# Performance work log

Measured on AMD Instinct MI355X. Metric: run time of the kernel, lower is better.

The kernel has to match this reference:

```python
import jax, jax.numpy as jnp
import numpy as np

B, T, K = 256, 64, 512


def setup_inputs() -> dict:
    key = jax.random.key(0)
    k1, k2, k3, k4, k5 = jax.random.split(key, 5)
    return {
        "x": jax.random.uniform(k1, (B, T), dtype=jnp.float32),          # soft binary evidence
        "prior_w": jax.random.normal(k2, (K,), dtype=jnp.float32),
        "emission_w": jax.random.normal(k3, (K, 2), dtype=jnp.float32),
        "coeff": jax.random.normal(k4, (K, K), dtype=jnp.float32),
        "bias": jax.random.normal(k5, (K, K), dtype=jnp.float32),
    }


def reference(x, prior_w, emission_w, coeff, bias):
    # emission: per-row softmax of [K,2] raw weights (TF loops rows; equivalent to axis=1 softmax)
    emission = jax.nn.softmax(emission_w, axis=1)  # [K, 2]

    def evidence(h, xt):
        # h: [B,K] (or broadcastable [1,K]); xt: [B]
        aug = jnp.stack([1.0 - xt, xt], axis=1)          # [B, 2]
        e = aug @ emission.T                             # [B, K]
        p = h * e                                        # [B, K]
        return p / jnp.sum(p, axis=1, keepdims=True)     # row-normalize (get_normalized_pr)

    prior = jax.nn.softmax(prior_w)                      # [K]
    post0 = evidence(prior[None, :], x[:, 0])            # [B, K]

    def step(post, xt):
        # transition_raw[i,j,k] = post[i,j]*coeff[j,k] + bias[j,k]
        raw = post[:, :, None] * coeff[None, :, :] + bias[None, :, :]   # [B, K, K]
        trans = jax.nn.softmax(raw, axis=2)              # get_normalized_pr_with_batch
        pbe = jnp.einsum('ij,ijk->ik', post, trans)      # [B, K]
        return evidence(pbe, xt), None

    post, _ = jax.lax.scan(step, post0, x[:, 1:].T)      # scan over time steps 1..T-1
    return post
```

## Files before the change

kernel.cpp:

```cpp
#include <hip/hip_runtime.h>

#define KDIM 512
#define TDIM 64
#define NWAVE 16
#define BLOCK 1024
#define LOG2E 1.4426950408889634f

typedef float v2f __attribute__((ext_vector_type(2)));

#define WS_B2     0
#define WS_XCHG   (KDIM * KDIM)
#define WS_FLAGS  (WS_XCHG + 128 * 2 * 2 * 1024)
#define WS_FLOATS (WS_FLAGS + 256)

__device__ __forceinline__ float fast_exp2(float v) { return __builtin_amdgcn_exp2f(v); }
__device__ __forceinline__ float fast_rcp(float v)  { return __builtin_amdgcn_rcpf(v); }

__global__ __launch_bounds__(256) void prefold_kernel(
    const float* __restrict__ bias, float* __restrict__ b2)
{
    const int i = blockIdx.x * 256 + threadIdx.x;
    const float4 b = ((const float4*)bias)[i];
    ((float4*)b2)[i] = make_float4(b.x * LOG2E, b.y * LOG2E, b.z * LOG2E, b.w * LOG2E);
}

__device__ __forceinline__ float wave_reduce_sum(float v) {
    #pragma unroll
    for (int off = 1; off < 64; off <<= 1)
        v += __shfl_xor(v, off, 64);
    return v;
}

__global__ __launch_bounds__(BLOCK)
__attribute__((amdgpu_waves_per_eu(4, 4)))
void hmm_pair_kernel(
    const float* __restrict__ x,
    const float* __restrict__ prior_w,
    const float* __restrict__ emission_w,
    const float* __restrict__ coeff,
    float* __restrict__ ws,
    float* __restrict__ out)
{
    __shared__ float post[2][KDIM];
    __shared__ float em0s[KDIM];
    __shared__ float emds[KDIM];
    __shared__ float part[NWAVE][2][KDIM];
    __shared__ float rtmp[NWAVE];
    __shared__ float xs[2][TDIM];

    const int gid  = blockIdx.x;
    const int pair = gid & 127;
    const int h    = gid >> 7;
    const int b0   = 2 * pair;
    const int tid  = threadIdx.x;
    const int lane = tid & 63;
    const int wv   = tid >> 6;
    const int k0   = 4 * lane;
    const int u    = tid >> 9;
    const int k    = tid & 511;

    const float* bb = ws + WS_B2;
    int* flags   = (int*)(ws + WS_FLAGS);
    int* my_flag = flags + (pair * 2 + h);
    int* pr_flag = flags + (pair * 2 + (1 - h));
    float* my_slot = ws + WS_XCHG + (size_t)(pair * 2 + h) * 2048;
    float* pr_slot = ws + WS_XCHG + (size_t)(pair * 2 + (1 - h)) * 2048;

    if (tid < 2 * TDIM) xs[tid >> 6][tid & 63] = x[(b0 + (tid >> 6)) * TDIM + (tid & 63)];
    if (tid < KDIM) {
        const float w0 = emission_w[2 * tid + 0];
        const float w1 = emission_w[2 * tid + 1];
        const float e0 = 1.0f / (1.0f + fast_exp2((w1 - w0) * LOG2E));
        em0s[tid] = e0;
        emds[tid] = 1.0f - 2.0f * e0;
    }
    __syncthreads();

    {
        const float x0 = xs[u][0];
        float v = fast_exp2(prior_w[k] * LOG2E) * fmaf(x0, emds[k], em0s[k]);
        float s = wave_reduce_sum(v);
        if (lane == 0) rtmp[wv] = s;
        __syncthreads();
        const float* rb = &rtmp[u * 8];
        const float tot = ((rb[0] + rb[1]) + (rb[2] + rb[3]))
                        + ((rb[4] + rb[5]) + (rb[6] + rb[7]));
        post[u][k] = v * fast_rcp(tot);
        __syncthreads();
    }

    for (int t = 1; t < TDIM; ++t) {
        v2f acc[2][4];
        #pragma unroll
        for (int uu = 0; uu < 2; ++uu)
            #pragma unroll
            for (int q = 0; q < 4; ++q) acc[uu][q] = (v2f){0.0f, 0.0f};

        const float* pc = coeff + (size_t)(h * 256 + wv) * KDIM + k0;
        const float* pb = bb    + (size_t)(h * 256 + wv) * KDIM + k0;

        #pragma unroll 1
        for (int i = 0; i < 8; ++i) {
            const int jA = h * 256 + wv + 32 * i;
            const float4 cA0 = *(const float4*)pc;
            const float4 cA1 = *(const float4*)(pc + 256);
            const float4 cB0 = *(const float4*)(pc + 16 * KDIM);
            const float4 cB1 = *(const float4*)(pc + 16 * KDIM + 256);
            const float4 bA0 = *(const float4*)pb;
            const float4 bA1 = *(const float4*)(pb + 256);
            const float4 bB0 = *(const float4*)(pb + 16 * KDIM);
            const float4 bB1 = *(const float4*)(pb + 16 * KDIM + 256);
            pc += 32 * KDIM; pb += 32 * KDIM;

            const v2f cav[4] = {{cA0.x, cA0.y}, {cA0.z, cA0.w}, {cA1.x, cA1.y}, {cA1.z, cA1.w}};
            const v2f cbv[4] = {{cB0.x, cB0.y}, {cB0.z, cB0.w}, {cB1.x, cB1.y}, {cB1.z, cB1.w}};
            const v2f bav[4] = {{bA0.x, bA0.y}, {bA0.z, bA0.w}, {bA1.x, bA1.y}, {bA1.z, bA1.w}};
            const v2f bbv[4] = {{bB0.x, bB0.y}, {bB0.z, bB0.w}, {bB1.x, bB1.y}, {bB1.z, bB1.w}};

            float p[2][2];
            p[0][0] = post[0][jA]; p[0][1] = post[0][jA + 16];
            p[1][0] = post[1][jA]; p[1][1] = post[1][jA + 16];

            v2f ev[2][2][4];
            float s[4];
            #pragma unroll
            for (int uu = 0; uu < 2; ++uu) {
                const float pAL = p[uu][0] * LOG2E;
                const float pBL = p[uu][1] * LOG2E;
                const v2f pAv = {pAL, pAL};
                const v2f pBv = {pBL, pBL};
                #pragma unroll
                for (int q = 0; q < 4; ++q) {
                    const v2f aA = __builtin_elementwise_fma(pAv, cav[q], bav[q]);
                    const v2f aB = __builtin_elementwise_fma(pBv, cbv[q], bbv[q]);
                    v2f eA, eB;
                    eA.x = fast_exp2(aA.x); eA.y = fast_exp2(aA.y);
                    eB.x = fast_exp2(aB.x); eB.y = fast_exp2(aB.y);
                    ev[uu][0][q] = eA;
                    ev[uu][1][q] = eB;
                }
                const v2f tA = (ev[uu][0][0] + ev[uu][0][1]) + (ev[uu][0][2] + ev[uu][0][3]);
                const v2f tB = (ev[uu][1][0] + ev[uu][1][1]) + (ev[uu][1][2] + ev[uu][1][3]);
                s[uu * 2 + 0] = tA.x + tA.y;
                s[uu * 2 + 1] = tB.x + tB.y;
            }
            #pragma unroll
            for (int off = 1; off < 64; off <<= 1) {
                s[0] += __shfl_xor(s[0], off, 64);
                s[1] += __shfl_xor(s[1], off, 64);
                s[2] += __shfl_xor(s[2], off, 64);
                s[3] += __shfl_xor(s[3], off, 64);
            }
            #pragma unroll
            for (int uu = 0; uu < 2; ++uu) {
                const float scA = p[uu][0] * fast_rcp(s[uu * 2 + 0]);
                const float scB = p[uu][1] * fast_rcp(s[uu * 2 + 1]);
                const v2f scAv = {scA, scA};
                const v2f scBv = {scB, scB};
                #pragma unroll
                for (int q = 0; q < 4; ++q) {
                    acc[uu][q] = __builtin_elementwise_fma(scAv, ev[uu][0][q], acc[uu][q]);
                    acc[uu][q] = __builtin_elementwise_fma(scBv, ev[uu][1][q], acc[uu][q]);
                }
            }
        }

        *(float4*)(&part[wv][0][k0])       = make_float4(acc[0][0].x, acc[0][0].y, acc[0][1].x, acc[0][1].y);
        *(float4*)(&part[wv][0][256 + k0]) = make_float4(acc[0][2].x, acc[0][2].y, acc[0][3].x, acc[0][3].y);
        *(float4*)(&part[wv][1][k0])       = make_float4(acc[1][0].x, acc[1][0].y, acc[1][1].x, acc[1][1].y);
        *(float4*)(&part[wv][1][256 + k0]) = make_float4(acc[1][2].x, acc[1][2].y, acc[1][3].x, acc[1][3].y);
        __syncthreads();

        float pbe = 0.0f;
        #pragma unroll
        for (int w2 = 0; w2 < NWAVE; ++w2) pbe += part[w2][u][k];

        float* slot = my_slot + (t & 1) * 1024;
        __hip_atomic_store(&slot[tid], pbe, __ATOMIC_RELAXED, __HIP_MEMORY_SCOPE_AGENT);
        __syncthreads();
        if (tid == 0) {
            __hip_atomic_store(my_flag, t, __ATOMIC_RELEASE, __HIP_MEMORY_SCOPE_AGENT);
            int f = __hip_atomic_load(pr_flag, __ATOMIC_ACQUIRE, __HIP_MEMORY_SCOPE_AGENT);
            while (f < t) {
                __builtin_amdgcn_s_sleep(1);
                f = __hip_atomic_load(pr_flag, __ATOMIC_ACQUIRE, __HIP_MEMORY_SCOPE_AGENT);
            }
        }
        __syncthreads();
        const float* pslot = pr_slot + (t & 1) * 1024;
        const float other = __hip_atomic_load(&pslot[tid], __ATOMIC_RELAXED, __HIP_MEMORY_SCOPE_AGENT);

        float v = (pbe + other) * fmaf(xs[u][t], emds[k], em0s[k]);
        float s = wave_reduce_sum(v);
        if (lane == 0) rtmp[wv] = s;
        __syncthreads();
        const float* rb = &rtmp[u * 8];
        const float tot = ((rb[0] + rb[1]) + (rb[2] + rb[3]))
                        + ((rb[4] + rb[5]) + (rb[6] + rb[7]));
        post[u][k] = v * fast_rcp(tot);
        __syncthreads();
    }

    if (tid < KDIM) out[(size_t)(b0 + h) * KDIM + tid] = post[h][tid];
}

__global__ __launch_bounds__(BLOCK)
__attribute__((amdgpu_waves_per_eu(4, 4)))
void hmm_forward_kernel(
    const float* __restrict__ x, const float* __restrict__ prior_w,
    const float* __restrict__ emission_w, const float* __restrict__ coeff,
    const float* __restrict__ bias, float* __restrict__ out)
{
    __shared__ float post[KDIM];
    __shared__ float em0s[KDIM];
    __shared__ float emds[KDIM];
    __shared__ float part[NWAVE][KDIM];
    __shared__ float rtmp[NWAVE];
    __shared__ float xs[TDIM];

    const int b = blockIdx.x, tid = threadIdx.x, lane = tid & 63, wv = tid >> 6;
    const int k0 = 4 * lane;

    if (tid < TDIM) xs[tid] = x[b * TDIM + tid];
    if (tid < KDIM) {
        const float w0 = emission_w[2 * tid + 0];
        const float w1 = emission_w[2 * tid + 1];
        const float e0 = 1.0f / (1.0f + fast_exp2((w1 - w0) * LOG2E));
        em0s[tid] = e0;
        emds[tid] = 1.0f - 2.0f * e0;
    }
    __syncthreads();
    {
        const float x0 = xs[0];
        float v = 0.0f;
        if (tid < KDIM)
            v = fast_exp2(prior_w[tid] * LOG2E) * fmaf(x0, emds[tid], em0s[tid]);
        float s = wave_reduce_sum(v);
        if (lane == 0) rtmp[wv] = s;
        __syncthreads();
        if (wv == 0) {
            float t2 = (lane < NWAVE) ? rtmp[lane] : 0.0f;
            #pragma unroll
            for (int off = 1; off < NWAVE; off <<= 1) t2 += __shfl_xor(t2, off, 64);
            if (lane == 0) rtmp[0] = t2;
        }
        __syncthreads();
        const float rn = fast_rcp(rtmp[0]);
        if (tid < KDIM) post[tid] = v * rn;
        __syncthreads();
    }
    for (int t = 1; t < TDIM; ++t) {
        float acc[8];
        #pragma unroll
        for (int i = 0; i < 8; ++i) acc[i] = 0.0f;
        const float* cA = coeff + (size_t)wv * KDIM + k0;
        const float* bA = bias  + (size_t)wv * KDIM + k0;
        #pragma unroll 1
        for (int i = 0; i < 16; ++i) {
            const float4 cA0 = *(const float4*)cA;
            const float4 cA1 = *(const float4*)(cA + 256);
            const float4 cB0 = *(const float4*)(cA + 16 * KDIM);
            const float4 cB1 = *(const float4*)(cA + 16 * KDIM + 256);
            const float4 bA0 = *(const float4*)bA;
            const float4 bA1 = *(const float4*)(bA + 256);
            const float4 bB0 = *(const float4*)(bA + 16 * KDIM);
            const float4 bB1 = *(const float4*)(bA + 16 * KDIM + 256);
            cA += 32 * KDIM; bA += 32 * KDIM;
            const float pA = post[wv + 32 * i];
            const float pB = post[wv + 16 + 32 * i];
            const float eA0 = fast_exp2(fmaf(pA, cA0.x, bA0.x) * LOG2E);
            const float eA1 = fast_exp2(fmaf(pA, cA0.y, bA0.y) * LOG2E);
            const float eA2 = fast_exp2(fmaf(pA, cA0.z, bA0.z) * LOG2E);
            const float eA3 = fast_exp2(fmaf(pA, cA0.w, bA0.w) * LOG2E);
            const float eA4 = fast_exp2(fmaf(pA, cA1.x, bA1.x) * LOG2E);
            const float eA5 = fast_exp2(fmaf(pA, cA1.y, bA1.y) * LOG2E);
            const float eA6 = fast_exp2(fmaf(pA, cA1.z, bA1.z) * LOG2E);
            const float eA7 = fast_exp2(fmaf(pA, cA1.w, bA1.w) * LOG2E);
            const float eB0 = fast_exp2(fmaf(pB, cB0.x, bB0.x) * LOG2E);
            const float eB1 = fast_exp2(fmaf(pB, cB0.y, bB0.y) * LOG2E);
            const float eB2 = fast_exp2(fmaf(pB, cB0.z, bB0.z) * LOG2E);
            const float eB3 = fast_exp2(fmaf(pB, cB0.w, bB0.w) * LOG2E);
            const float eB4 = fast_exp2(fmaf(pB, cB1.x, bB1.x) * LOG2E);
            const float eB5 = fast_exp2(fmaf(pB, cB1.y, bB1.y) * LOG2E);
            const float eB6 = fast_exp2(fmaf(pB, cB1.z, bB1.z) * LOG2E);
            const float eB7 = fast_exp2(fmaf(pB, cB1.w, bB1.w) * LOG2E);
            float sA = ((eA0 + eA1) + (eA2 + eA3)) + ((eA4 + eA5) + (eA6 + eA7));
            float sB = ((eB0 + eB1) + (eB2 + eB3)) + ((eB4 + eB5) + (eB6 + eB7));
            #pragma unroll
            for (int off = 1; off < 64; off <<= 1) {
                sA += __shfl_xor(sA, off, 64);
                sB += __shfl_xor(sB, off, 64);
            }
            const float scA = pA * fast_rcp(sA);
            const float scB = pB * fast_rcp(sB);
            acc[0] = fmaf(scA, eA0, acc[0]); acc[0] = fmaf(scB, eB0, acc[0]);
            acc[1] = fmaf(scA, eA1, acc[1]); acc[1] = fmaf(scB, eB1, acc[1]);
            acc[2] = fmaf(scA, eA2, acc[2]); acc[2] = fmaf(scB, eB2, acc[2]);
            acc[3] = fmaf(scA, eA3, acc[3]); acc[3] = fmaf(scB, eB3, acc[3]);
            acc[4] = fmaf(scA, eA4, acc[4]); acc[4] = fmaf(scB, eB4, acc[4]);
            acc[5] = fmaf(scA, eA5, acc[5]); acc[5] = fmaf(scB, eB5, acc[5]);
            acc[6] = fmaf(scA, eA6, acc[6]); acc[6] = fmaf(scB, eB6, acc[6]);
            acc[7] = fmaf(scA, eA7, acc[7]); acc[7] = fmaf(scB, eB7, acc[7]);
        }
        *(float4*)(&part[wv][k0])       = make_float4(acc[0], acc[1], acc[2], acc[3]);
        *(float4*)(&part[wv][256 + k0]) = make_float4(acc[4], acc[5], acc[6], acc[7]);
        __syncthreads();
        float v = 0.0f;
        if (tid < KDIM) {
            float pbe = 0.0f;
            #pragma unroll
            for (int w2 = 0; w2 < NWAVE; ++w2) pbe += part[w2][tid];
            v = pbe * fmaf(xs[t], emds[tid], em0s[tid]);
        }
        float s = wave_reduce_sum(v);
        if (lane == 0) rtmp[wv] = s;
        __syncthreads();
        if (wv == 0) {
            float t2 = (lane < NWAVE) ? rtmp[lane] : 0.0f;
            #pragma unroll
            for (int off = 1; off < NWAVE; off <<= 1) t2 += __shfl_xor(t2, off, 64);
            if (lane == 0) rtmp[0] = t2;
        }
        __syncthreads();
        const float rn = fast_rcp(rtmp[0]);
        if (tid < KDIM) post[tid] = v * rn;
        __syncthreads();
    }
    if (tid < KDIM) out[b * KDIM + tid] = post[tid];
}

extern "C" void kernel_launch(void* const* d_in, const int* in_sizes, int n_in,
                              void* d_out, int out_size, void* d_ws, size_t ws_size,
                              hipStream_t stream) {
    const float* x          = (const float*)d_in[0];
    const float* prior_w    = (const float*)d_in[1];
    const float* emission_w = (const float*)d_in[2];
    const float* coeff      = (const float*)d_in[3];
    const float* bias       = (const float*)d_in[4];
    float* out              = (float*)d_out;

    if (ws_size >= (size_t)WS_FLOATS * sizeof(float)) {
        float* ws = (float*)d_ws;
        hipLaunchKernelGGL(prefold_kernel, dim3(KDIM * KDIM / 4 / 256), dim3(256),
                           0, stream, bias, ws + WS_B2);
        hipLaunchKernelGGL(hmm_pair_kernel, dim3(256), dim3(BLOCK), 0, stream,
                           x, prior_w, emission_w, coeff, ws, out);
    } else {
        hipLaunchKernelGGL(hmm_forward_kernel, dim3(256), dim3(BLOCK), 0, stream,
                           x, prior_w, emission_w, coeff, bias, out);
    }
}
```

Measured before the change: 1.134 ms.

## Split each batch row across two 512-thread blocks and use DPP reductions

The paired kernel previously had one 1024-thread block handle half of the j-range for two batch rows. Now each of 512 blocks handles one batch row and half of the j-range, and exchanges partial sums with a partner block through flags in the workspace. This doubles the grid so more CUs take part, and halves per-block register and LDS pressure. Wave reductions now use DPP row shifts instead of a full shuffle-xor ladder. The cost is that coeff and bias are re-read per row instead of shared across two rows, and twice as many cross-block flag syncs run per step.

```diff
diff --git a/kernel.cpp b/kernel.cpp
--- a/kernel.cpp
+++ b/kernel.cpp
@@ -2,19 +2,47 @@
 
 #define KDIM 512
 #define TDIM 64
-#define NWAVE 16
-#define BLOCK 1024
+#define BLOCK 512
+#define NWAVE 8
 #define LOG2E 1.4426950408889634f
 
 typedef float v2f __attribute__((ext_vector_type(2)));
 
 #define WS_B2     0
 #define WS_XCHG   (KDIM * KDIM)
-#define WS_FLAGS  (WS_XCHG + 128 * 2 * 2 * 1024)
-#define WS_FLOATS (WS_FLAGS + 256)
+#define WS_FLAGS  (WS_XCHG + 512 * 1024)
+#define WS_FLOATS (WS_FLAGS + 512)
 
 __device__ __forceinline__ float fast_exp2(float v) { return __builtin_amdgcn_exp2f(v); }
 __device__ __forceinline__ float fast_rcp(float v)  { return __builtin_amdgcn_rcpf(v); }
+
+template <int CTRL>
+__device__ __forceinline__ float dpp_add(float v) {
+    const int p = __builtin_amdgcn_update_dpp(
+        0, __builtin_bit_cast(int, v), CTRL, 0xF, 0xF, true);
+    return v + __builtin_bit_cast(float, p);
+}
+
+__device__ __forceinline__ float row_sum64(float v) {
+    v = dpp_add<0x121>(v);
+    v = dpp_add<0x122>(v);
+    v = dpp_add<0x124>(v);
+    v = dpp_add<0x128>(v);
+    v += __shfl_xor(v, 16, 64);
+    v += __shfl_xor(v, 32, 64);
+    return v;
+}
+
+__device__ __forceinline__ void row_sum64_x2(float& a, float& b) {
+    a = dpp_add<0x121>(a); b = dpp_add<0x121>(b);
+    a = dpp_add<0x122>(a); b = dpp_add<0x122>(b);
+    a = dpp_add<0x124>(a); b = dpp_add<0x124>(b);
+    a = dpp_add<0x128>(a); b = dpp_add<0x128>(b);
+    float ta = __shfl_xor(a, 16, 64), tb = __shfl_xor(b, 16, 64);
+    a += ta; b += tb;
+    ta = __shfl_xor(a, 32, 64); tb = __shfl_xor(b, 32, 64);
+    a += ta; b += tb;
+}
 
 __global__ __launch_bounds__(256) void prefold_kernel(
     const float* __restrict__ bias, float* __restrict__ b2)
@@ -22,13 +50,6 @@
     const int i = blockIdx.x * 256 + threadIdx.x;
     const float4 b = ((const float4*)bias)[i];
     ((float4*)b2)[i] = make_float4(b.x * LOG2E, b.y * LOG2E, b.z * LOG2E, b.w * LOG2E);
-}
-
-__device__ __forceinline__ float wave_reduce_sum(float v) {
-    #pragma unroll
-    for (int off = 1; off < 64; off <<= 1)
-        v += __shfl_xor(v, off, 64);
-    return v;
 }
 
 __global__ __launch_bounds__(BLOCK)
@@ -41,33 +62,30 @@
     float* __restrict__ ws,
     float* __restrict__ out)
 {
-    __shared__ float post[2][KDIM];
+    __shared__ float post[KDIM];
     __shared__ float em0s[KDIM];
     __shared__ float emds[KDIM];
-    __shared__ float part[NWAVE][2][KDIM];
+    __shared__ float part[NWAVE][KDIM];
     __shared__ float rtmp[NWAVE];
-    __shared__ float xs[2][TDIM];
+    __shared__ float xs[TDIM];
 
     const int gid  = blockIdx.x;
-    const int pair = gid & 127;
-    const int h    = gid >> 7;
-    const int b0   = 2 * pair;
+    const int b    = gid & 255;
+    const int h    = gid >> 8;
     const int tid  = threadIdx.x;
     const int lane = tid & 63;
     const int wv   = tid >> 6;
     const int k0   = 4 * lane;
-    const int u    = tid >> 9;
-    const int k    = tid & 511;
 
     const float* bb = ws + WS_B2;
     int* flags   = (int*)(ws + WS_FLAGS);
-    int* my_flag = flags + (pair * 2 + h);
-    int* pr_flag = flags + (pair * 2 + (1 - h));
-    float* my_slot = ws + WS_XCHG + (size_t)(pair * 2 + h) * 2048;
-    float* pr_slot = ws + WS_XCHG + (size_t)(pair * 2 + (1 - h)) * 2048;
-
-    if (tid < 2 * TDIM) xs[tid >> 6][tid & 63] = x[(b0 + (tid >> 6)) * TDIM + (tid & 63)];
-    if (tid < KDIM) {
+    int* my_flag = flags + (b * 2 + h);
+    int* pr_flag = flags + (b * 2 + (1 - h));
+    float* my_slot = ws + WS_XCHG + (size_t)(b * 2 + h) * 1024;
+    float* pr_slot = ws + WS_XCHG + (size_t)(b * 2 + (1 - h)) * 1024;
+
+    if (tid < TDIM) xs[tid] = x[b * TDIM + tid];
+    {
         const float w0 = emission_w[2 * tid + 0];
         const float w1 = emission_w[2 * tid + 1];
         const float e0 = 1.0f / (1.0f + fast_exp2((w1 - w0) * LOG2E));
@@ -77,105 +95,83 @@
     __syncthreads();
 
     {
-        const float x0 = xs[u][0];
-        float v = fast_exp2(prior_w[k] * LOG2E) * fmaf(x0, emds[k], em0s[k]);
-        float s = wave_reduce_sum(v);
+        const float x0 = xs[0];
+        float v = fast_exp2(prior_w[tid] * LOG2E) * fmaf(x0, emds[tid], em0s[tid]);
+        const float s = row_sum64(v);
         if (lane == 0) rtmp[wv] = s;
         __syncthreads();
-        const float* rb = &rtmp[u * 8];
-        const float tot = ((rb[0] + rb[1]) + (rb[2] + rb[3]))
-                        + ((rb[4] + rb[5]) + (rb[6] + rb[7]));
-        post[u][k] = v * fast_rcp(tot);
+        const float tot = ((rtmp[0] + rtmp[1]) + (rtmp[2] + rtmp[3]))
+                        + ((rtmp[4] + rtmp[5]) + (rtmp[6] + rtmp[7]));
+        post[tid] = v * fast_rcp(tot);
         __syncthreads();
     }
 
     for (int t = 1; t < TDIM; ++t) {
-        v2f acc[2][4];
+        v2f acc[4];
         #pragma unroll
-        for (int uu = 0; uu < 2; ++uu)
-            #pragma unroll
-            for (int q = 0; q < 4; ++q) acc[uu][q] = (v2f){0.0f, 0.0f};
+        for (int q = 0; q < 4; ++q) acc[q] = (v2f){0.0f, 0.0f};
 
         const float* pc = coeff + (size_t)(h * 256 + wv) * KDIM + k0;
         const float* pb = bb    + (size_t)(h * 256 + wv) * KDIM + k0;
 
         #pragma unroll 1
-        for (int i = 0; i < 8; ++i) {
-            const int jA = h * 256 + wv + 32 * i;
+        for (int i = 0; i < 16; ++i) {
+            const int jA = h * 256 + wv + 16 * i;
             const float4 cA0 = *(const float4*)pc;
             const float4 cA1 = *(const float4*)(pc + 256);
-            const float4 cB0 = *(const float4*)(pc + 16 * KDIM);
-            const float4 cB1 = *(const float4*)(pc + 16 * KDIM + 256);
+            const float4 cB0 = *(const float4*)(pc + 8 * KDIM);
+            const float4 cB1 = *(const float4*)(pc + 8 * KDIM + 256);
             const float4 bA0 = *(const float4*)pb;
             const float4 bA1 = *(const float4*)(pb + 256);
-            const float4 bB0 = *(const float4*)(pb + 16 * KDIM);
-            const float4 bB1 = *(const float4*)(pb + 16 * KDIM + 256);
-            pc += 32 * KDIM; pb += 32 * KDIM;
+            const float4 bB0 = *(const float4*)(pb + 8 * KDIM);
+            const float4 bB1 = *(const float4*)(pb + 8 * KDIM + 256);
+            pc += 16 * KDIM; pb += 16 * KDIM;
 
             const v2f cav[4] = {{cA0.x, cA0.y}, {cA0.z, cA0.w}, {cA1.x, cA1.y}, {cA1.z, cA1.w}};
             const v2f cbv[4] = {{cB0.x, cB0.y}, {cB0.z, cB0.w}, {cB1.x, cB1.y}, {cB1.z, cB1.w}};
             const v2f bav[4] = {{bA0.x, bA0.y}, {bA0.z, bA0.w}, {bA1.x, bA1.y}, {bA1.z, bA1.w}};
             const v2f bbv[4] = {{bB0.x, bB0.y}, {bB0.z, bB0.w}, {bB1.x, bB1.y}, {bB1.z, bB1.w}};
 
-            float p[2][2];
-            p[0][0] = post[0][jA]; p[0][1] = post[0][jA + 16];
-            p[1][0] = post[1][jA]; p[1][1] = post[1][jA + 16];
-
-            v2f ev[2][2][4];
-            float s[4];
+            const float pA = post[jA];
+            const float pB = post[jA + 8];
+            const float pAL = pA * LOG2E;
+            const float pBL = pB * LOG2E;
+            const v2f pAv = {pAL, pAL};
+            const v2f pBv = {pBL, pBL};
+
+            v2f eA[4], eB[4];
             #pragma unroll
-            for (int uu = 0; uu < 2; ++uu) {
-                const float pAL = p[uu][0] * LOG2E;
-                const float pBL = p[uu][1] * LOG2E;
-                const v2f pAv = {pAL, pAL};
-                const v2f pBv = {pBL, pBL};
-                #pragma unroll
-                for (int q = 0; q < 4; ++q) {
-                    const v2f aA = __builtin_elementwise_fma(pAv, cav[q], bav[q]);
-                    const v2f aB = __builtin_elementwise_fma(pBv, cbv[q], bbv[q]);
-                    v2f eA, eB;
-                    eA.x = fast_exp2(aA.x); eA.y = fast_exp2(aA.y);
-                    eB.x = fast_exp2(aB.x); eB.y = fast_exp2(aB.y);
-                    ev[uu][0][q] = eA;
-                    ev[uu][1][q] = eB;
-                }
-                const v2f tA = (ev[uu][0][0] + ev[uu][0][1]) + (ev[uu][0][2] + ev[uu][0][3]);
-                const v2f tB = (ev[uu][1][0] + ev[uu][1][1]) + (ev[uu][1][2] + ev[uu][1][3]);
-                s[uu * 2 + 0] = tA.x + tA.y;
-                s[uu * 2 + 1] = tB.x + tB.y;
+            for (int q = 0; q < 4; ++q) {
+                const v2f aA = __builtin_elementwise_fma(pAv, cav[q], bav[q]);
+                const v2f aB = __builtin_elementwise_fma(pBv, cbv[q], bbv[q]);
+                eA[q].x = fast_exp2(aA.x); eA[q].y = fast_exp2(aA.y);
+                eB[q].x = fast_exp2(aB.x); eB[q].y = fast_exp2(aB.y);
             }
+            const v2f tA = (eA[0] + eA[1]) + (eA[2] + eA[3]);
+            const v2f tB = (eB[0] + eB[1]) + (eB[2] + eB[3]);
+            float sA = tA.x + tA.y;
+            float sB = tB.x + tB.y;
+            row_sum64_x2(sA, sB);
+
+            const float scA = pA * fast_rcp(sA);
+            const float scB = pB * fast_rcp(sB);
+            const v2f scAv = {scA, scA};
+            const v2f scBv = {scB, scB};
             #pragma unroll
-            for (int off = 1; off < 64; off <<= 1) {
-                s[0] += __shfl_xor(s[0], off, 64);
-                s[1] += __shfl_xor(s[1], off, 64);
-                s[2] += __shfl_xor(s[2], off, 64);
-                s[3] += __shfl_xor(s[3], off, 64);
-            }
-            #pragma unroll
-            for (int uu = 0; uu < 2; ++uu) {
-                const float scA = p[uu][0] * fast_rcp(s[uu * 2 + 0]);
-                const float scB = p[uu][1] * fast_rcp(s[uu * 2 + 1]);
-                const v2f scAv = {scA, scA};
-                const v2f scBv = {scB, scB};
-                #pragma unroll
-                for (int q = 0; q < 4; ++q) {
-                    acc[uu][q] = __builtin_elementwise_fma(scAv, ev[uu][0][q], acc[uu][q]);
-                    acc[uu][q] = __builtin_elementwise_fma(scBv, ev[uu][1][q], acc[uu][q]);
-                }
+            for (int q = 0; q < 4; ++q) {
+                acc[q] = __builtin_elementwise_fma(scAv, eA[q], acc[q]);
+                acc[q] = __builtin_elementwise_fma(scBv, eB[q], acc[q]);
             }
         }
 
-        *(float4*)(&part[wv][0][k0])       = make_float4(acc[0][0].x, acc[0][0].y, acc[0][1].x, acc[0][1].y);
-        *(float4*)(&part[wv][0][256 + k0]) = make_float4(acc[0][2].x, acc[0][2].y, acc[0][3].x, acc[0][3].y);
-        *(float4*)(&part[wv][1][k0])       = make_float4(acc[1][0].x, acc[1][0].y, acc[1][1].x, acc[1][1].y);
-        *(float4*)(&part[wv][1][256 + k0]) = make_float4(acc[1][2].x, acc[1][2].y, acc[1][3].x, acc[1][3].y);
-        __syncthreads();
-
-        float pbe = 0.0f;
-        #pragma unroll
-        for (int w2 = 0; w2 < NWAVE; ++w2) pbe += part[w2][u][k];
-
-        float* slot = my_slot + (t & 1) * 1024;
+        *(float4*)(&part[wv][k0])       = make_float4(acc[0].x, acc[0].y, acc[1].x, acc[1].y);
+        *(float4*)(&part[wv][256 + k0]) = make_float4(acc[2].x, acc[2].y, acc[3].x, acc[3].y);
+        __syncthreads();
+
+        float pbe = ((part[0][tid] + part[1][tid]) + (part[2][tid] + part[3][tid]))
+                  + ((part[4][tid] + part[5][tid]) + (part[6][tid] + part[7][tid]));
+
+        float* slot = my_slot + (t & 1) * 512;
         __hip_atomic_store(&slot[tid], pbe, __ATOMIC_RELAXED, __HIP_MEMORY_SCOPE_AGENT);
         __syncthreads();
         if (tid == 0) {
@@ -187,24 +183,23 @@
             }
         }
         __syncthreads();
-        const float* pslot = pr_slot + (t & 1) * 1024;
+        const float* pslot = pr_slot + (t & 1) * 512;
         const float other = __hip_atomic_load(&pslot[tid], __ATOMIC_RELAXED, __HIP_MEMORY_SCOPE_AGENT);
 
-        float v = (pbe + other) * fmaf(xs[u][t], emds[k], em0s[k]);
-        float s = wave_reduce_sum(v);
+        float v = (pbe + other) * fmaf(xs[t], emds[tid], em0s[tid]);
+        const float s = row_sum64(v);
         if (lane == 0) rtmp[wv] = s;
         __syncthreads();
-        const float* rb = &rtmp[u * 8];
-        const float tot = ((rb[0] + rb[1]) + (rb[2] + rb[3]))
-                        + ((rb[4] + rb[5]) + (rb[6] + rb[7]));
-        post[u][k] = v * fast_rcp(tot);
-        __syncthreads();
-    }
-
-    if (tid < KDIM) out[(size_t)(b0 + h) * KDIM + tid] = post[h][tid];
-}
-
-__global__ __launch_bounds__(BLOCK)
+        const float tot = ((rtmp[0] + rtmp[1]) + (rtmp[2] + rtmp[3]))
+                        + ((rtmp[4] + rtmp[5]) + (rtmp[6] + rtmp[7]));
+        post[tid] = v * fast_rcp(tot);
+        __syncthreads();
+    }
+
+    if (h == 0) out[(size_t)b * KDIM + tid] = post[tid];
+}
+
+__global__ __launch_bounds__(1024)
 __attribute__((amdgpu_waves_per_eu(4, 4)))
 void hmm_forward_kernel(
     const float* __restrict__ x, const float* __restrict__ prior_w,
@@ -214,8 +209,8 @@
     __shared__ float post[KDIM];
     __shared__ float em0s[KDIM];
     __shared__ float emds[KDIM];
-    __shared__ float part[NWAVE][KDIM];
-    __shared__ float rtmp[NWAVE];
+    __shared__ float part[16][KDIM];
+    __shared__ float rtmp[16];
     __shared__ float xs[TDIM];
 
     const int b = blockIdx.x, tid = threadIdx.x, lane = tid & 63, wv = tid >> 6;
@@ -235,18 +230,13 @@
         float v = 0.0f;
         if (tid < KDIM)
             v = fast_exp2(prior_w[tid] * LOG2E) * fmaf(x0, emds[tid], em0s[tid]);
-        float s = wave_reduce_sum(v);
+        float s = row_sum64(v);
         if (lane == 0) rtmp[wv] = s;
         __syncthreads();
-        if (wv == 0) {
-            float t2 = (lane < NWAVE) ? rtmp[lane] : 0.0f;
-            #pragma unroll
-            for (int off = 1; off < NWAVE; off <<= 1) t2 += __shfl_xor(t2, off, 64);
-            if (lane == 0) rtmp[0] = t2;
-        }
-        __syncthreads();
-        const float rn = fast_rcp(rtmp[0]);
-        if (tid < KDIM) post[tid] = v * rn;
+        float tot = 0.0f;
+        #pragma unroll
+        for (int w2 = 0; w2 < 16; ++w2) tot += rtmp[w2];
+        if (tid < KDIM) post[tid] = v * fast_rcp(tot);
         __syncthreads();
     }
     for (int t = 1; t < TDIM; ++t) {
@@ -286,11 +276,7 @@
             const float eB7 = fast_exp2(fmaf(pB, cB1.w, bB1.w) * LOG2E);
             float sA = ((eA0 + eA1) + (eA2 + eA3)) + ((eA4 + eA5) + (eA6 + eA7));
             float sB = ((eB0 + eB1) + (eB2 + eB3)) + ((eB4 + eB5) + (eB6 + eB7));
-            #pragma unroll
-            for (int off = 1; off < 64; off <<= 1) {
-                sA += __shfl_xor(sA, off, 64);
-                sB += __shfl_xor(sB, off, 64);
-            }
+            row_sum64_x2(sA, sB);
             const float scA = pA * fast_rcp(sA);
             const float scB = pB * fast_rcp(sB);
             acc[0] = fmaf(scA, eA0, acc[0]); acc[0] = fmaf(scB, eB0, acc[0]);
@@ -309,21 +295,16 @@
         if (tid < KDIM) {
             float pbe = 0.0f;
             #pragma unroll
-            for (int w2 = 0; w2 < NWAVE; ++w2) pbe += part[w2][tid];
+            for (int w2 = 0; w2 < 16; ++w2) pbe += part[w2][tid];
             v = pbe * fmaf(xs[t], emds[tid], em0s[tid]);
         }
-        float s = wave_reduce_sum(v);
+        float s = row_sum64(v);
         if (lane == 0) rtmp[wv] = s;
         __syncthreads();
-        if (wv == 0) {
-            float t2 = (lane < NWAVE) ? rtmp[lane] : 0.0f;
-            #pragma unroll
-            for (int off = 1; off < NWAVE; off <<= 1) t2 += __shfl_xor(t2, off, 64);
-            if (lane == 0) rtmp[0] = t2;
-        }
-        __syncthreads();
-        const float rn = fast_rcp(rtmp[0]);
-        if (tid < KDIM) post[tid] = v * rn;
+        float tot = 0.0f;
+        #pragma unroll
+        for (int w2 = 0; w2 < 16; ++w2) tot += rtmp[w2];
+        if (tid < KDIM) post[tid] = v * fast_rcp(tot);
         __syncthreads();
     }
     if (tid < KDIM) out[b * KDIM + tid] = post[tid];
@@ -343,10 +324,10 @@
         float* ws = (float*)d_ws;
         hipLaunchKernelGGL(prefold_kernel, dim3(KDIM * KDIM / 4 / 256), dim3(256),
                            0, stream, bias, ws + WS_B2);
-        hipLaunchKernelGGL(hmm_pair_kernel, dim3(256), dim3(BLOCK), 0, stream,
+        hipLaunchKernelGGL(hmm_pair_kernel, dim3(512), dim3(BLOCK), 0, stream,
                            x, prior_w, emission_w, coeff, ws, out);
     } else {
-        hipLaunchKernelGGL(hmm_forward_kernel, dim3(256), dim3(BLOCK), 0, stream,
+        hipLaunchKernelGGL(hmm_forward_kernel, dim3(256), dim3(1024), 0, stream,
                            x, prior_w, emission_w, coeff, bias, out);
     }
 }
```

New measurement: 3.812 ms. 236% more time.

## Use DPP row reductions and per-wave cross-block flags instead of block barriers

Applied to the files above, without the earlier changes.

Wave-wide sums now use DPP row-shift adds for the first four reduction steps and shuffles only for the last two, which shortens the reduction chain inside the hot softmax loop. The pair-exchange handshake switches to one flag per wave: each wave publishes and polls its own flag with relaxed loads and an acquire fence. This removes the two block-wide barriers around the cross-block exchange. It adds more flag traffic and spinning waves, and the flag workspace is enlarged to hold the per-wave flags.

```diff
diff --git a/kernel.cpp b/kernel.cpp
--- a/kernel.cpp
+++ b/kernel.cpp
@@ -10,11 +10,45 @@
 
 #define WS_B2     0
 #define WS_XCHG   (KDIM * KDIM)
-#define WS_FLAGS  (WS_XCHG + 128 * 2 * 2 * 1024)
-#define WS_FLOATS (WS_FLAGS + 256)
+#define WS_FLAGS  (WS_XCHG + 256 * 2048)
+#define WS_FLOATS (WS_FLAGS + 128 * 2 * 16)
 
 __device__ __forceinline__ float fast_exp2(float v) { return __builtin_amdgcn_exp2f(v); }
 __device__ __forceinline__ float fast_rcp(float v)  { return __builtin_amdgcn_rcpf(v); }
+
+template <int CTRL>
+__device__ __forceinline__ float dpp_add(float v) {
+    const int p = __builtin_amdgcn_update_dpp(
+        0, __builtin_bit_cast(int, v), CTRL, 0xF, 0xF, true);
+    return v + __builtin_bit_cast(float, p);
+}
+
+__device__ __forceinline__ float row_sum64(float v) {
+    v = dpp_add<0x121>(v);
+    v = dpp_add<0x122>(v);
+    v = dpp_add<0x124>(v);
+    v = dpp_add<0x128>(v);
+    v += __shfl_xor(v, 16, 64);
+    v += __shfl_xor(v, 32, 64);
+    return v;
+}
+
+__device__ __forceinline__ void row_sum64_x4(float* s) {
+    #pragma unroll
+    for (int q = 0; q < 4; ++q) s[q] = dpp_add<0x121>(s[q]);
+    #pragma unroll
+    for (int q = 0; q < 4; ++q) s[q] = dpp_add<0x122>(s[q]);
+    #pragma unroll
+    for (int q = 0; q < 4; ++q) s[q] = dpp_add<0x124>(s[q]);
+    #pragma unroll
+    for (int q = 0; q < 4; ++q) s[q] = dpp_add<0x128>(s[q]);
+    float t0 = __shfl_xor(s[0], 16, 64), t1 = __shfl_xor(s[1], 16, 64);
+    float t2 = __shfl_xor(s[2], 16, 64), t3 = __shfl_xor(s[3], 16, 64);
+    s[0] += t0; s[1] += t1; s[2] += t2; s[3] += t3;
+    t0 = __shfl_xor(s[0], 32, 64); t1 = __shfl_xor(s[1], 32, 64);
+    t2 = __shfl_xor(s[2], 32, 64); t3 = __shfl_xor(s[3], 32, 64);
+    s[0] += t0; s[1] += t1; s[2] += t2; s[3] += t3;
+}
 
 __global__ __launch_bounds__(256) void prefold_kernel(
     const float* __restrict__ bias, float* __restrict__ b2)
@@ -22,13 +56,6 @@
     const int i = blockIdx.x * 256 + threadIdx.x;
     const float4 b = ((const float4*)bias)[i];
     ((float4*)b2)[i] = make_float4(b.x * LOG2E, b.y * LOG2E, b.z * LOG2E, b.w * LOG2E);
-}
-
-__device__ __forceinline__ float wave_reduce_sum(float v) {
-    #pragma unroll
-    for (int off = 1; off < 64; off <<= 1)
-        v += __shfl_xor(v, off, 64);
-    return v;
 }
 
 __global__ __launch_bounds__(BLOCK)
@@ -61,8 +88,8 @@
 
     const float* bb = ws + WS_B2;
     int* flags   = (int*)(ws + WS_FLAGS);
-    int* my_flag = flags + (pair * 2 + h);
-    int* pr_flag = flags + (pair * 2 + (1 - h));
+    int* my_flag = flags + ((pair * 2 + h) * 16 + wv);
+    int* pr_flag = flags + ((pair * 2 + (1 - h)) * 16 + wv);
     float* my_slot = ws + WS_XCHG + (size_t)(pair * 2 + h) * 2048;
     float* pr_slot = ws + WS_XCHG + (size_t)(pair * 2 + (1 - h)) * 2048;
 
@@ -79,7 +106,7 @@
     {
         const float x0 = xs[u][0];
         float v = fast_exp2(prior_w[k] * LOG2E) * fmaf(x0, emds[k], em0s[k]);
-        float s = wave_reduce_sum(v);
+        const float s = row_sum64(v);
         if (lane == 0) rtmp[wv] = s;
         __syncthreads();
         const float* rb = &rtmp[u * 8];
@@ -144,13 +171,8 @@
                 s[uu * 2 + 0] = tA.x + tA.y;
                 s[uu * 2 + 1] = tB.x + tB.y;
             }
-            #pragma unroll
-            for (int off = 1; off < 64; off <<= 1) {
-                s[0] += __shfl_xor(s[0], off, 64);
-                s[1] += __shfl_xor(s[1], off, 64);
-                s[2] += __shfl_xor(s[2], off, 64);
-                s[3] += __shfl_xor(s[3], off, 64);
-            }
+            row_sum64_x4(s);
+
             #pragma unroll
             for (int uu = 0; uu < 2; ++uu) {
                 const float scA = p[uu][0] * fast_rcp(s[uu * 2 + 0]);
@@ -177,21 +199,19 @@
 
         float* slot = my_slot + (t & 1) * 1024;
         __hip_atomic_store(&slot[tid], pbe, __ATOMIC_RELAXED, __HIP_MEMORY_SCOPE_AGENT);
-        __syncthreads();
-        if (tid == 0) {
+        if (lane == 0)
             __hip_atomic_store(my_flag, t, __ATOMIC_RELEASE, __HIP_MEMORY_SCOPE_AGENT);
-            int f = __hip_atomic_load(pr_flag, __ATOMIC_ACQUIRE, __HIP_MEMORY_SCOPE_AGENT);
-            while (f < t) {
-                __builtin_amdgcn_s_sleep(1);
-                f = __hip_atomic_load(pr_flag, __ATOMIC_ACQUIRE, __HIP_MEMORY_SCOPE_AGENT);
-            }
+        int f = __hip_atomic_load(pr_flag, __ATOMIC_RELAXED, __HIP_MEMORY_SCOPE_AGENT);
+        while (f < t) {
+            __builtin_amdgcn_s_sleep(4);
+            f = __hip_atomic_load(pr_flag, __ATOMIC_RELAXED, __HIP_MEMORY_SCOPE_AGENT);
         }
-        __syncthreads();
+        __builtin_amdgcn_fence(__ATOMIC_ACQUIRE, "agent");
         const float* pslot = pr_slot + (t & 1) * 1024;
         const float other = __hip_atomic_load(&pslot[tid], __ATOMIC_RELAXED, __HIP_MEMORY_SCOPE_AGENT);
 
         float v = (pbe + other) * fmaf(xs[u][t], emds[k], em0s[k]);
-        float s = wave_reduce_sum(v);
+        const float s = row_sum64(v);
         if (lane == 0) rtmp[wv] = s;
         __syncthreads();
         const float* rb = &rtmp[u * 8];
@@ -204,7 +224,7 @@
     if (tid < KDIM) out[(size_t)(b0 + h) * KDIM + tid] = post[h][tid];
 }
 
-__global__ __launch_bounds__(BLOCK)
+__global__ __launch_bounds__(1024)
 __attribute__((amdgpu_waves_per_eu(4, 4)))
 void hmm_forward_kernel(
     const float* __restrict__ x, const float* __restrict__ prior_w,
@@ -214,8 +234,8 @@
     __shared__ float post[KDIM];
     __shared__ float em0s[KDIM];
     __shared__ float emds[KDIM];
-    __shared__ float part[NWAVE][KDIM];
-    __shared__ float rtmp[NWAVE];
+    __shared__ float part[16][KDIM];
+    __shared__ float rtmp[16];
     __shared__ float xs[TDIM];
 
     const int b = blockIdx.x, tid = threadIdx.x, lane = tid & 63, wv = tid >> 6;
@@ -235,18 +255,13 @@
         float v = 0.0f;
         if (tid < KDIM)
             v = fast_exp2(prior_w[tid] * LOG2E) * fmaf(x0, emds[tid], em0s[tid]);
-        float s = wave_reduce_sum(v);
+        float s = row_sum64(v);
         if (lane == 0) rtmp[wv] = s;
         __syncthreads();
-        if (wv == 0) {
-            float t2 = (lane < NWAVE) ? rtmp[lane] : 0.0f;
-            #pragma unroll
-            for (int off = 1; off < NWAVE; off <<= 1) t2 += __shfl_xor(t2, off, 64);
-            if (lane == 0) rtmp[0] = t2;
-        }
-        __syncthreads();
-        const float rn = fast_rcp(rtmp[0]);
-        if (tid < KDIM) post[tid] = v * rn;
+        float tot = 0.0f;
+        #pragma unroll
+        for (int w2 = 0; w2 < 16; ++w2) tot += rtmp[w2];
+        if (tid < KDIM) post[tid] = v * fast_rcp(tot);
         __syncthreads();
     }
     for (int t = 1; t < TDIM; ++t) {
@@ -268,6 +283,7 @@
             cA += 32 * KDIM; bA += 32 * KDIM;
             const float pA = post[wv + 32 * i];
             const float pB = post[wv + 16 + 32 * i];
+            float s4[4];
             const float eA0 = fast_exp2(fmaf(pA, cA0.x, bA0.x) * LOG2E);
             const float eA1 = fast_exp2(fmaf(pA, cA0.y, bA0.y) * LOG2E);
             const float eA2 = fast_exp2(fmaf(pA, cA0.z, bA0.z) * LOG2E);
@@ -284,15 +300,12 @@
             const float eB5 = fast_exp2(fmaf(pB, cB1.y, bB1.y) * LOG2E);
             const float eB6 = fast_exp2(fmaf(pB, cB1.z, bB1.z) * LOG2E);
             const float eB7 = fast_exp2(fmaf(pB, cB1.w, bB1.w) * LOG2E);
-            float sA = ((eA0 + eA1) + (eA2 + eA3)) + ((eA4 + eA5) + (eA6 + eA7));
-            float sB = ((eB0 + eB1) + (eB2 + eB3)) + ((eB4 + eB5) + (eB6 + eB7));
-            #pragma unroll
-            for (int off = 1; off < 64; off <<= 1) {
-                sA += __shfl_xor(sA, off, 64);
-                sB += __shfl_xor(sB, off, 64);
-            }
-            const float scA = pA * fast_rcp(sA);
-            const float scB = pB * fast_rcp(sB);
+            s4[0] = ((eA0 + eA1) + (eA2 + eA3)) + ((eA4 + eA5) + (eA6 + eA7));
+            s4[1] = ((eB0 + eB1) + (eB2 + eB3)) + ((eB4 + eB5) + (eB6 + eB7));
+            s4[2] = 0.0f; s4[3] = 0.0f;
+            row_sum64_x4(s4);
+            const float scA = pA * fast_rcp(s4[0]);
+            const float scB = pB * fast_rcp(s4[1]);
             acc[0] = fmaf(scA, eA0, acc[0]); acc[0] = fmaf(scB, eB0, acc[0]);
             acc[1] = fmaf(scA, eA1, acc[1]); acc[1] = fmaf(scB, eB1, acc[1]);
             acc[2] = fmaf(scA, eA2, acc[2]); acc[2] = fmaf(scB, eB2, acc[2]);
@@ -309,21 +322,16 @@
         if (tid < KDIM) {
             float pbe = 0.0f;
             #pragma unroll
-            for (int w2 = 0; w2 < NWAVE; ++w2) pbe += part[w2][tid];
+            for (int w2 = 0; w2 < 16; ++w2) pbe += part[w2][tid];
             v = pbe * fmaf(xs[t], emds[tid], em0s[tid]);
         }
-        float s = wave_reduce_sum(v);
+        float s = row_sum64(v);
         if (lane == 0) rtmp[wv] = s;
         __syncthreads();
-        if (wv == 0) {
-            float t2 = (lane < NWAVE) ? rtmp[lane] : 0.0f;
-            #pragma unroll
-            for (int off = 1; off < NWAVE; off <<= 1) t2 += __shfl_xor(t2, off, 64);
-            if (lane == 0) rtmp[0] = t2;
-        }
-        __syncthreads();
-        const float rn = fast_rcp(rtmp[0]);
-        if (tid < KDIM) post[tid] = v * rn;
+        float tot = 0.0f;
+        #pragma unroll
+        for (int w2 = 0; w2 < 16; ++w2) tot += rtmp[w2];
+        if (tid < KDIM) post[tid] = v * fast_rcp(tot);
         __syncthreads();
     }
     if (tid < KDIM) out[b * KDIM + tid] = post[tid];
@@ -346,7 +354,7 @@
         hipLaunchKernelGGL(hmm_pair_kernel, dim3(256), dim3(BLOCK), 0, stream,
                            x, prior_w, emission_w, coeff, ws, out);
     } else {
-        hipLaunchKernelGGL(hmm_forward_kernel, dim3(256), dim3(BLOCK), 0, stream,
+        hipLaunchKernelGGL(hmm_forward_kernel, dim3(256), dim3(1024), 0, stream,
                            x, prior_w, emission_w, coeff, bias, out);
     }
 }
```

After: 4.466 ms. 3.94x slower.
